# Optimization experiments

Hardware: AMD Instinct MI355X
Metric: run time of the kernel (lower is better)

## Reference

```python
import jax, jax.numpy as jnp
import numpy as np

DIM = 256
B, N, M = 4, 4096, 8


def setup_inputs() -> dict:
    key = jax.random.key(0)
    ks = jax.random.split(key, 12)
    s = 1.0 / np.sqrt(DIM)
    return {
        "q": jax.random.normal(ks[0], (B, DIM, N, M), jnp.float32),
        "k": jax.random.normal(ks[1], (B, DIM, N, M), jnp.float32),
        "pos": jax.random.normal(ks[2], (B, N, M, DIM), jnp.float32),
        "mask": jnp.ones((B, N, M, 1), jnp.int32),
        "Wq": jax.random.normal(ks[3], (DIM, DIM), jnp.float32) * s,
        "Wk": jax.random.normal(ks[4], (DIM, DIM), jnp.float32) * s,
        "Wv": jax.random.normal(ks[5], (DIM, DIM), jnp.float32) * s,
        "W1": jax.random.normal(ks[6], (DIM, DIM // 2), jnp.float32) * s,
        "b1": jnp.zeros((DIM // 2,), jnp.float32),
        "W2": jax.random.normal(ks[7], (DIM // 2, DIM), jnp.float32) * s,
        "b2": jnp.zeros((DIM,), jnp.float32),
        "Wo": jax.random.normal(ks[8], (DIM, DIM), jnp.float32) * s,
        "bo": jnp.zeros((DIM,), jnp.float32),
    }


def reference(q, k, pos, mask, Wq, Wk, Wv, W1, b1, W2, b2, Wo, bo):
    # (B, dim, N, M) -> (B, N, M, dim)
    qh = jnp.einsum('bdnm,de->bnme', q, Wq)
    kh = jnp.einsum('bdnm,de->bnme', k, Wk)
    v = kh @ Wv  # note: v_fc applied to k_fc output, as in the original
    attn = kh - qh + pos
    attn = jax.nn.relu(attn @ W1 + b1) @ W2 + b2
    attn = jnp.where(mask == 0, -1e9, attn)
    attn = jax.nn.sigmoid(attn)
    x = (v + pos) * attn
    x = x @ Wo + bo
    return jnp.transpose(x, (0, 3, 1, 2))  # back to (B, dim, N, M)
```

## Files before the change

### kernel.cpp

```cpp
#include <hip/hip_runtime.h>

#define DIMX 256
#define NMX  32768
#define TB   64

typedef short s16x8 __attribute__((ext_vector_type(8)));
typedef float f32x4 __attribute__((ext_vector_type(4)));

#define OFF_WQN   (0u)
#define OFF_WK    (131072u)
#define OFF_WKV   (262144u)
#define OFF_W1    (393216u)
#define OFF_W2    (458752u)
#define OFF_WO    (524288u)
#define OFF_KVF32 (655360u)

__device__ __forceinline__ ushort f2bf(float f) {
  uint u = __builtin_bit_cast(uint, f);
  return (ushort)((u + 0x7FFFu + ((u >> 16) & 1u)) >> 16);
}

__global__ void wkv_kernel(const float* __restrict__ Wk, const float* __restrict__ Wv,
                           float* __restrict__ outw) {
  const int e = threadIdx.x, d = blockIdx.x;
  float acc = 0.f;
  #pragma unroll 8
  for (int m = 0; m < DIMX; ++m) acc += Wk[d * DIMX + m] * Wv[m * DIMX + e];
  outw[d * DIMX + e] = acc;
}

__global__ void pack_kernel(const float* __restrict__ Wq, const float* __restrict__ Wk,
                            const float* __restrict__ Wkvf, const float* __restrict__ W1,
                            const float* __restrict__ W2, const float* __restrict__ Wo,
                            ushort* __restrict__ wsout) {
  const int fid = blockIdx.x, lane = threadIdx.x;
  const float* src; int Eout = 256; float sgn = 1.f; uint off; int local;
  if (fid < 128)      { src = Wq;   sgn = -1.f; off = OFF_WQN; local = fid;       }
  else if (fid < 256) { src = Wk;   off = OFF_WK;  local = fid - 128;             }
  else if (fid < 384) { src = Wkvf; off = OFF_WKV; local = fid - 256;             }
  else if (fid < 448) { src = W1;   Eout = 128; off = OFF_W1; local = fid - 384;  }
  else if (fid < 512) { src = W2;   off = OFF_W2;  local = fid - 448;             }
  else                { src = Wo;   off = OFF_WO;  local = fid - 512;             }
  const int R  = Eout >> 4;
  const int ks = local / R, r = local - ks * R;
  const int e  = r * 16 + (lane & 15);
  const int k0 = ks * 32 + (lane >> 4) * 8;
  union { uint4 u4; ushort us[8]; } o;
  #pragma unroll
  for (int j = 0; j < 8; ++j) o.us[j] = f2bf(sgn * src[(k0 + j) * Eout + e]);
  *(uint4*)((char*)wsout + off + (((uint)local * 64u + (uint)lane) * 16u)) = o.u4;
}

#define MFMA16(A,B,C) __builtin_amdgcn_mfma_f32_16x16x32_bf16(A, B, C, 0, 0, 0)

__global__ __launch_bounds__(512, 4) void fused_main(
    const float* __restrict__ q, const float* __restrict__ kin,
    const float* __restrict__ pos, const int* __restrict__ mask,
    const float* __restrict__ b1, const float* __restrict__ b2,
    const float* __restrict__ bo, const ushort* __restrict__ wfr,
    float* __restrict__ out)
{
  __shared__ __align__(1024) ushort bufA[TB * DIMX];
  __shared__ __align__(1024) ushort bufB[TB * DIMX];
  const char* wb = (const char*)wfr;

  const int tid = threadIdx.x;
  const int w = tid >> 6, l = tid & 63;
  const int c = l & 15, g = l >> 4;
  const int b  = blockIdx.x >> 9;
  const int t0 = (blockIdx.x & 511) * TB;

  auto ldB = [&](const ushort* buf, int ks, int tf) -> s16x8 {
    const int t = (tf << 4) + c;
    const int col = (ks << 6) + (g << 4);
    return *(const s16x8*)((const char*)buf + t * 512 + (col ^ ((t & 7) << 4)));
  };
  auto ldA = [&](uint moff, int fi) -> s16x8 {
    return *(const s16x8*)(wb + moff + (((uint)fi << 6) | (uint)l) * 16u);
  };
  auto stRow4 = [&](ushort* buf, int e0, int t, uint lo, uint hi) {
    const int byte = t * 512 + (((uint)(e0 * 2)) ^ ((t & 7) << 4));
    *(uint2*)((char*)buf + byte) = uint2{lo, hi};
  };

  {
    const size_t pbase = (size_t)b * DIMX * NMX + t0 + l;
    #pragma unroll 4
    for (int dd = 0; dd < 32; dd += 2) {
      const int d = (w << 5) + dd;
      const float q0 = q[pbase + (size_t)d * NMX];
      const float q1 = q[pbase + (size_t)(d + 1) * NMX];
      const float k0 = kin[pbase + (size_t)d * NMX];
      const float k1 = kin[pbase + (size_t)(d + 1) * NMX];
      const int byte = l * 512 + ((d * 2) ^ ((l & 7) << 4));
      *(uint*)((char*)bufA + byte) = (uint)f2bf(q0) | ((uint)f2bf(q1) << 16);
      *(uint*)((char*)bufB + byte) = (uint)f2bf(k0) | ((uint)f2bf(k1) << 16);
    }
  }
  __syncthreads();

  f32x4 av[2][4];
  #pragma unroll
  for (int ef = 0; ef < 2; ++ef)
    #pragma unroll
    for (int tf = 0; tf < 4; ++tf) av[ef][tf] = f32x4{0.f, 0.f, 0.f, 0.f};
  #pragma unroll 2
  for (int ks = 0; ks < 8; ++ks) {
    const s16x8 a0 = ldA(OFF_WKV, (ks << 4) + (w << 1));
    const s16x8 a1 = ldA(OFF_WKV, (ks << 4) + (w << 1) + 1);
    #pragma unroll
    for (int tf = 0; tf < 4; ++tf) {
      const s16x8 bf = ldB(bufB, ks, tf);
      av[0][tf] = MFMA16(a0, bf, av[0][tf]);
      av[1][tf] = MFMA16(a1, bf, av[1][tf]);
    }
  }
  uint vbf[2][4][2];
  #pragma unroll
  for (int ef = 0; ef < 2; ++ef)
    #pragma unroll
    for (int tf = 0; tf < 4; ++tf)
      #pragma unroll
      for (int p = 0; p < 2; ++p)
        vbf[ef][tf][p] = (uint)f2bf(av[ef][tf][2 * p]) |
                         ((uint)f2bf(av[ef][tf][2 * p + 1]) << 16);

  f32x4 aa[2][4];
  #pragma unroll
  for (int ef = 0; ef < 2; ++ef)
    #pragma unroll
    for (int tf = 0; tf < 4; ++tf) aa[ef][tf] = f32x4{0.f, 0.f, 0.f, 0.f};
  #pragma unroll 2
  for (int ks = 0; ks < 8; ++ks) {
    const s16x8 a0 = ldA(OFF_WQN, (ks << 4) + (w << 1));
    const s16x8 a1 = ldA(OFF_WQN, (ks << 4) + (w << 1) + 1);
    #pragma unroll
    for (int tf = 0; tf < 4; ++tf) {
      const s16x8 bf = ldB(bufA, ks, tf);
      aa[0][tf] = MFMA16(a0, bf, aa[0][tf]);
      aa[1][tf] = MFMA16(a1, bf, aa[1][tf]);
    }
  }
  #pragma unroll 2
  for (int ks = 0; ks < 8; ++ks) {
    const s16x8 a0 = ldA(OFF_WK, (ks << 4) + (w << 1));
    const s16x8 a1 = ldA(OFF_WK, (ks << 4) + (w << 1) + 1);
    #pragma unroll
    for (int tf = 0; tf < 4; ++tf) {
      const s16x8 bf = ldB(bufB, ks, tf);
      aa[0][tf] = MFMA16(a0, bf, aa[0][tf]);
      aa[1][tf] = MFMA16(a1, bf, aa[1][tf]);
    }
  }
  __syncthreads();

  #pragma unroll
  for (int tf = 0; tf < 4; ++tf) {
    const int t = (tf << 4) + c;
    const float* pp = pos + ((size_t)b * NMX + t0 + t) * DIMX;
    #pragma unroll
    for (int ef = 0; ef < 2; ++ef) {
      const int e0 = (w << 5) + (ef << 4) + (g << 2);
      const f32x4 p4 = *(const f32x4*)(pp + e0);
      const uint lo = (uint)f2bf(aa[ef][tf][0] + p4[0]) |
                      ((uint)f2bf(aa[ef][tf][1] + p4[1]) << 16);
      const uint hi = (uint)f2bf(aa[ef][tf][2] + p4[2]) |
                      ((uint)f2bf(aa[ef][tf][3] + p4[3]) << 16);
      stRow4(bufA, e0, t, lo, hi);
    }
  }
  __syncthreads();

  f32x4 ah[4];
  #pragma unroll
  for (int tf = 0; tf < 4; ++tf) ah[tf] = f32x4{0.f, 0.f, 0.f, 0.f};
  #pragma unroll 2
  for (int ks = 0; ks < 8; ++ks) {
    const s16x8 a0 = ldA(OFF_W1, (ks << 3) + w);
    #pragma unroll
    for (int tf = 0; tf < 4; ++tf) {
      const s16x8 bf = ldB(bufA, ks, tf);
      ah[tf] = MFMA16(a0, bf, ah[tf]);
    }
  }
  {
    const int e0 = (w << 4) + (g << 2);
    const f32x4 b1v = *(const f32x4*)(b1 + e0);
    #pragma unroll
    for (int tf = 0; tf < 4; ++tf) {
      const int t = (tf << 4) + c;
      const uint lo = (uint)f2bf(fmaxf(ah[tf][0] + b1v[0], 0.f)) |
                      ((uint)f2bf(fmaxf(ah[tf][1] + b1v[1], 0.f)) << 16);
      const uint hi = (uint)f2bf(fmaxf(ah[tf][2] + b1v[2], 0.f)) |
                      ((uint)f2bf(fmaxf(ah[tf][3] + b1v[3], 0.f)) << 16);
      stRow4(bufB, e0, t, lo, hi);
    }
  }
  __syncthreads();

  f32x4 as[2][4];
  #pragma unroll
  for (int ef = 0; ef < 2; ++ef)
    #pragma unroll
    for (int tf = 0; tf < 4; ++tf) as[ef][tf] = f32x4{0.f, 0.f, 0.f, 0.f};
  #pragma unroll
  for (int ks = 0; ks < 4; ++ks) {
    const s16x8 a0 = ldA(OFF_W2, (ks << 4) + (w << 1));
    const s16x8 a1 = ldA(OFF_W2, (ks << 4) + (w << 1) + 1);
    #pragma unroll
    for (int tf = 0; tf < 4; ++tf) {
      const s16x8 bf = ldB(bufB, ks, tf);
      as[0][tf] = MFMA16(a0, bf, as[0][tf]);
      as[1][tf] = MFMA16(a1, bf, as[1][tf]);
    }
  }
  #pragma unroll
  for (int tf = 0; tf < 4; ++tf) {
    const int t = (tf << 4) + c;
    const int mk = mask[(size_t)b * NMX + t0 + t];
    const float* pp = pos + ((size_t)b * NMX + t0 + t) * DIMX;
    #pragma unroll
    for (int ef = 0; ef < 2; ++ef) {
      const int e0 = (w << 5) + (ef << 4) + (g << 2);
      const f32x4 p4  = *(const f32x4*)(pp + e0);
      const f32x4 b2v = *(const f32x4*)(b2 + e0);
      float xv[4];
      #pragma unroll
      for (int i = 0; i < 4; ++i) {
        float sv = as[ef][tf][i] + b2v[i];
        if (mk == 0) sv = -1e9f;
        const float sig = 1.f / (1.f + __expf(-sv));
        const uint pv = vbf[ef][tf][i >> 1];
        const float vv = (i & 1) ? __builtin_bit_cast(float, pv & 0xffff0000u)
                                 : __builtin_bit_cast(float, pv << 16);
        xv[i] = (vv + p4[i]) * sig;
      }
      const uint lo = (uint)f2bf(xv[0]) | ((uint)f2bf(xv[1]) << 16);
      const uint hi = (uint)f2bf(xv[2]) | ((uint)f2bf(xv[3]) << 16);
      stRow4(bufA, e0, t, lo, hi);
    }
  }
  __syncthreads();

  f32x4 ao[2][4];
  #pragma unroll
  for (int ef = 0; ef < 2; ++ef)
    #pragma unroll
    for (int tf = 0; tf < 4; ++tf) ao[ef][tf] = f32x4{0.f, 0.f, 0.f, 0.f};
  #pragma unroll 2
  for (int ks = 0; ks < 8; ++ks) {
    const s16x8 a0 = ldA(OFF_WO, (ks << 4) + (w << 1));
    const s16x8 a1 = ldA(OFF_WO, (ks << 4) + (w << 1) + 1);
    #pragma unroll
    for (int tf = 0; tf < 4; ++tf) {
      const s16x8 bf = ldB(bufA, ks, tf);
      ao[0][tf] = MFMA16(a0, bf, ao[0][tf]);
      ao[1][tf] = MFMA16(a1, bf, ao[1][tf]);
    }
  }
  #pragma unroll
  for (int ef = 0; ef < 2; ++ef) {
    const int e0 = (w << 5) + (ef << 4) + (g << 2);
    const f32x4 bov = *(const f32x4*)(bo + e0);
    #pragma unroll
    for (int i = 0; i < 4; ++i) {
      float* ob = out + ((size_t)b * DIMX + e0 + i) * NMX + t0 + c;
      #pragma unroll
      for (int tf = 0; tf < 4; ++tf)
        ob[tf << 4] = ao[ef][tf][i] + bov[i];
    }
  }
}

extern "C" void kernel_launch(void* const* d_in, const int* in_sizes, int n_in,
                              void* d_out, int out_size, void* d_ws, size_t ws_size,
                              hipStream_t stream) {
  (void)in_sizes; (void)n_in; (void)out_size; (void)ws_size;
  const float* q   = (const float*)d_in[0];
  const float* k   = (const float*)d_in[1];
  const float* pos = (const float*)d_in[2];
  const int*   msk = (const int*)d_in[3];
  const float* Wq  = (const float*)d_in[4];
  const float* Wk  = (const float*)d_in[5];
  const float* Wv  = (const float*)d_in[6];
  const float* W1  = (const float*)d_in[7];
  const float* b1  = (const float*)d_in[8];
  const float* W2  = (const float*)d_in[9];
  const float* b2  = (const float*)d_in[10];
  const float* Wo  = (const float*)d_in[11];
  const float* bo  = (const float*)d_in[12];
  float* out = (float*)d_out;
  char* ws = (char*)d_ws;
  float*  wkvf = (float*)(ws + OFF_KVF32);
  ushort* wfr  = (ushort*)ws;

  wkv_kernel<<<dim3(256), dim3(256), 0, stream>>>(Wk, Wv, wkvf);
  pack_kernel<<<dim3(640), dim3(64), 0, stream>>>(Wq, Wk, wkvf, W1, W2, Wo, wfr);
  fused_main<<<dim3(2048), dim3(512), 0, stream>>>(q, k, pos, msk, b1, b2, bo, wfr, out);
}
```

Baseline: 206.1 us.

## Shrink LDS footprint by staging q in halves, raise occupancy, use hardware bf16 pack

Replaces the two 32KB LDS buffers with one 32KB main buffer and one 16KB auxiliary buffer. q is now staged in two 128-column halves, with an extra barrier between the halves, so more blocks can fit per CU; launch bounds go from 4 to 6 blocks. The software bf16 rounding is replaced with the v_cvt_pk_bf16_f32 instruction, and staging stores are widened to 16 bytes. pos is kept in registers as packed bf16 instead of being reloaded from global memory, which adds register pressure and slightly lowers the precision of pos in the final product.

```diff
diff --git a/kernel.cpp b/kernel.cpp
--- a/kernel.cpp
+++ b/kernel.cpp
@@ -18,6 +18,18 @@
 __device__ __forceinline__ ushort f2bf(float f) {
   uint u = __builtin_bit_cast(uint, f);
   return (ushort)((u + 0x7FFFu + ((u >> 16) & 1u)) >> 16);
+}
+
+__device__ __forceinline__ uint cvtpk(float lo, float hi) {
+  uint r;
+  asm("v_cvt_pk_bf16_f32 %0, %1, %2" : "=v"(r) : "v"(lo), "v"(hi));
+  return r;
+}
+__device__ __forceinline__ float bf_lo(uint u) {
+  return __builtin_bit_cast(float, u << 16);
+}
+__device__ __forceinline__ float bf_hi(uint u) {
+  return __builtin_bit_cast(float, u & 0xffff0000u);
 }
 
 __global__ void wkv_kernel(const float* __restrict__ Wk, const float* __restrict__ Wv,
@@ -53,15 +65,17 @@
 
 #define MFMA16(A,B,C) __builtin_amdgcn_mfma_f32_16x16x32_bf16(A, B, C, 0, 0, 0)
 
-__global__ __launch_bounds__(512, 4) void fused_main(
+__global__ __launch_bounds__(512, 6) void fused_main(
     const float* __restrict__ q, const float* __restrict__ kin,
     const float* __restrict__ pos, const int* __restrict__ mask,
     const float* __restrict__ b1, const float* __restrict__ b2,
     const float* __restrict__ bo, const ushort* __restrict__ wfr,
     float* __restrict__ out)
 {
-  __shared__ __align__(1024) ushort bufA[TB * DIMX];
-  __shared__ __align__(1024) ushort bufB[TB * DIMX];
+  __shared__ __align__(1024) ushort mainb[TB * DIMX];
+  __shared__ __align__(1024) ushort auxb[TB * (DIMX / 2)];
+  char* mb = (char*)mainb;
+  char* ab = (char*)auxb;
   const char* wb = (const char*)wfr;
 
   const int tid = threadIdx.x;
@@ -70,33 +84,64 @@
   const int b  = blockIdx.x >> 9;
   const int t0 = (blockIdx.x & 511) * TB;
 
-  auto ldB = [&](const ushort* buf, int ks, int tf) -> s16x8 {
+  auto ldBm = [&](int ks, int tf) -> s16x8 {
     const int t = (tf << 4) + c;
     const int col = (ks << 6) + (g << 4);
-    return *(const s16x8*)((const char*)buf + t * 512 + (col ^ ((t & 7) << 4)));
+    return *(const s16x8*)(mb + t * 512 + (col ^ ((t & 7) << 4)));
+  };
+  auto ldBa = [&](int ks, int tf) -> s16x8 {
+    const int t = (tf << 4) + c;
+    const int col = (ks << 6) + (g << 4);
+    return *(const s16x8*)(ab + t * 256 + (col ^ ((t & 7) << 4)));
   };
   auto ldA = [&](uint moff, int fi) -> s16x8 {
     return *(const s16x8*)(wb + moff + (((uint)fi << 6) | (uint)l) * 16u);
   };
-  auto stRow4 = [&](ushort* buf, int e0, int t, uint lo, uint hi) {
+  auto stM4 = [&](int e0, int t, uint lo, uint hi) {
     const int byte = t * 512 + (((uint)(e0 * 2)) ^ ((t & 7) << 4));
-    *(uint2*)((char*)buf + byte) = uint2{lo, hi};
-  };
-
-  {
-    const size_t pbase = (size_t)b * DIMX * NMX + t0 + l;
-    #pragma unroll 4
-    for (int dd = 0; dd < 32; dd += 2) {
-      const int d = (w << 5) + dd;
-      const float q0 = q[pbase + (size_t)d * NMX];
-      const float q1 = q[pbase + (size_t)(d + 1) * NMX];
-      const float k0 = kin[pbase + (size_t)d * NMX];
-      const float k1 = kin[pbase + (size_t)(d + 1) * NMX];
-      const int byte = l * 512 + ((d * 2) ^ ((l & 7) << 4));
-      *(uint*)((char*)bufA + byte) = (uint)f2bf(q0) | ((uint)f2bf(q1) << 16);
-      *(uint*)((char*)bufB + byte) = (uint)f2bf(k0) | ((uint)f2bf(k1) << 16);
-    }
-  }
+    *(uint2*)(mb + byte) = uint2{lo, hi};
+  };
+  auto stA4 = [&](int e0, int t, uint lo, uint hi) {
+    const int byte = t * 256 + (((uint)(e0 * 2)) ^ ((t & 7) << 4));
+    *(uint2*)(ab + byte) = uint2{lo, hi};
+  };
+
+  const size_t gbase = (size_t)b * DIMX * NMX + t0 + l;
+
+  auto stage_k = [&]() {
+    #pragma unroll
+    for (int j4 = 0; j4 < 4; ++j4) {
+      const int d0 = (w << 5) + (j4 << 3);
+      uint pk[4];
+      #pragma unroll
+      for (int p = 0; p < 4; ++p) {
+        const float v0 = kin[gbase + (size_t)(d0 + 2 * p) * NMX];
+        const float v1 = kin[gbase + (size_t)(d0 + 2 * p + 1) * NMX];
+        pk[p] = cvtpk(v0, v1);
+      }
+      const int byte = l * 512 + ((d0 * 2) ^ ((l & 7) << 4));
+      *(uint4*)(mb + byte) = uint4{pk[0], pk[1], pk[2], pk[3]};
+    }
+  };
+  auto stage_qh = [&](int half) {
+    #pragma unroll
+    for (int j4 = 0; j4 < 2; ++j4) {
+      const int dl = (w << 4) + (j4 << 3);
+      const int d  = (half << 7) + dl;
+      uint pk[4];
+      #pragma unroll
+      for (int p = 0; p < 4; ++p) {
+        const float v0 = q[gbase + (size_t)(d + 2 * p) * NMX];
+        const float v1 = q[gbase + (size_t)(d + 2 * p + 1) * NMX];
+        pk[p] = cvtpk(v0, v1);
+      }
+      const int byte = l * 256 + ((dl * 2) ^ ((l & 7) << 4));
+      *(uint4*)(ab + byte) = uint4{pk[0], pk[1], pk[2], pk[3]};
+    }
+  };
+
+  stage_k();
+  stage_qh(0);
   __syncthreads();
 
   f32x4 av[2][4];
@@ -110,7 +155,7 @@
     const s16x8 a1 = ldA(OFF_WKV, (ks << 4) + (w << 1) + 1);
     #pragma unroll
     for (int tf = 0; tf < 4; ++tf) {
-      const s16x8 bf = ldB(bufB, ks, tf);
+      const s16x8 bf = ldBm(ks, tf);
       av[0][tf] = MFMA16(a0, bf, av[0][tf]);
       av[1][tf] = MFMA16(a1, bf, av[1][tf]);
     }
@@ -119,41 +164,57 @@
   #pragma unroll
   for (int ef = 0; ef < 2; ++ef)
     #pragma unroll
-    for (int tf = 0; tf < 4; ++tf)
-      #pragma unroll
-      for (int p = 0; p < 2; ++p)
-        vbf[ef][tf][p] = (uint)f2bf(av[ef][tf][2 * p]) |
-                         ((uint)f2bf(av[ef][tf][2 * p + 1]) << 16);
+    for (int tf = 0; tf < 4; ++tf) {
+      vbf[ef][tf][0] = cvtpk(av[ef][tf][0], av[ef][tf][1]);
+      vbf[ef][tf][1] = cvtpk(av[ef][tf][2], av[ef][tf][3]);
+    }
 
   f32x4 aa[2][4];
   #pragma unroll
   for (int ef = 0; ef < 2; ++ef)
     #pragma unroll
     for (int tf = 0; tf < 4; ++tf) aa[ef][tf] = f32x4{0.f, 0.f, 0.f, 0.f};
-  #pragma unroll 2
-  for (int ks = 0; ks < 8; ++ks) {
-    const s16x8 a0 = ldA(OFF_WQN, (ks << 4) + (w << 1));
-    const s16x8 a1 = ldA(OFF_WQN, (ks << 4) + (w << 1) + 1);
-    #pragma unroll
-    for (int tf = 0; tf < 4; ++tf) {
-      const s16x8 bf = ldB(bufA, ks, tf);
-      aa[0][tf] = MFMA16(a0, bf, aa[0][tf]);
-      aa[1][tf] = MFMA16(a1, bf, aa[1][tf]);
-    }
-  }
   #pragma unroll 2
   for (int ks = 0; ks < 8; ++ks) {
     const s16x8 a0 = ldA(OFF_WK, (ks << 4) + (w << 1));
     const s16x8 a1 = ldA(OFF_WK, (ks << 4) + (w << 1) + 1);
     #pragma unroll
     for (int tf = 0; tf < 4; ++tf) {
-      const s16x8 bf = ldB(bufB, ks, tf);
+      const s16x8 bf = ldBm(ks, tf);
       aa[0][tf] = MFMA16(a0, bf, aa[0][tf]);
       aa[1][tf] = MFMA16(a1, bf, aa[1][tf]);
     }
   }
-  __syncthreads();
-
+
+  #pragma unroll 2
+  for (int ks = 0; ks < 4; ++ks) {
+    const s16x8 a0 = ldA(OFF_WQN, (ks << 4) + (w << 1));
+    const s16x8 a1 = ldA(OFF_WQN, (ks << 4) + (w << 1) + 1);
+    #pragma unroll
+    for (int tf = 0; tf < 4; ++tf) {
+      const s16x8 bf = ldBa(ks, tf);
+      aa[0][tf] = MFMA16(a0, bf, aa[0][tf]);
+      aa[1][tf] = MFMA16(a1, bf, aa[1][tf]);
+    }
+  }
+  __syncthreads();
+
+  stage_qh(1);
+  __syncthreads();
+
+  #pragma unroll 2
+  for (int ks = 4; ks < 8; ++ks) {
+    const s16x8 a0 = ldA(OFF_WQN, (ks << 4) + (w << 1));
+    const s16x8 a1 = ldA(OFF_WQN, (ks << 4) + (w << 1) + 1);
+    #pragma unroll
+    for (int tf = 0; tf < 4; ++tf) {
+      const s16x8 bf = ldBa(ks - 4, tf);
+      aa[0][tf] = MFMA16(a0, bf, aa[0][tf]);
+      aa[1][tf] = MFMA16(a1, bf, aa[1][tf]);
+    }
+  }
+
+  uint posbf[2][4][2];
   #pragma unroll
   for (int tf = 0; tf < 4; ++tf) {
     const int t = (tf << 4) + c;
@@ -162,11 +223,11 @@
     for (int ef = 0; ef < 2; ++ef) {
       const int e0 = (w << 5) + (ef << 4) + (g << 2);
       const f32x4 p4 = *(const f32x4*)(pp + e0);
-      const uint lo = (uint)f2bf(aa[ef][tf][0] + p4[0]) |
-                      ((uint)f2bf(aa[ef][tf][1] + p4[1]) << 16);
-      const uint hi = (uint)f2bf(aa[ef][tf][2] + p4[2]) |
-                      ((uint)f2bf(aa[ef][tf][3] + p4[3]) << 16);
-      stRow4(bufA, e0, t, lo, hi);
+      posbf[ef][tf][0] = cvtpk(p4[0], p4[1]);
+      posbf[ef][tf][1] = cvtpk(p4[2], p4[3]);
+      const uint lo = cvtpk(aa[ef][tf][0] + p4[0], aa[ef][tf][1] + p4[1]);
+      const uint hi = cvtpk(aa[ef][tf][2] + p4[2], aa[ef][tf][3] + p4[3]);
+      stM4(e0, t, lo, hi);
     }
   }
   __syncthreads();
@@ -179,7 +240,7 @@
     const s16x8 a0 = ldA(OFF_W1, (ks << 3) + w);
     #pragma unroll
     for (int tf = 0; tf < 4; ++tf) {
-      const s16x8 bf = ldB(bufA, ks, tf);
+      const s16x8 bf = ldBm(ks, tf);
       ah[tf] = MFMA16(a0, bf, ah[tf]);
     }
   }
@@ -189,11 +250,11 @@
     #pragma unroll
     for (int tf = 0; tf < 4; ++tf) {
       const int t = (tf << 4) + c;
-      const uint lo = (uint)f2bf(fmaxf(ah[tf][0] + b1v[0], 0.f)) |
-                      ((uint)f2bf(fmaxf(ah[tf][1] + b1v[1], 0.f)) << 16);
-      const uint hi = (uint)f2bf(fmaxf(ah[tf][2] + b1v[2], 0.f)) |
-                      ((uint)f2bf(fmaxf(ah[tf][3] + b1v[3], 0.f)) << 16);
-      stRow4(bufB, e0, t, lo, hi);
+      const uint lo = cvtpk(fmaxf(ah[tf][0] + b1v[0], 0.f),
+                            fmaxf(ah[tf][1] + b1v[1], 0.f));
+      const uint hi = cvtpk(fmaxf(ah[tf][2] + b1v[2], 0.f),
+                            fmaxf(ah[tf][3] + b1v[3], 0.f));
+      stA4(e0, t, lo, hi);
     }
   }
   __syncthreads();
@@ -209,7 +270,7 @@
     const s16x8 a1 = ldA(OFF_W2, (ks << 4) + (w << 1) + 1);
     #pragma unroll
     for (int tf = 0; tf < 4; ++tf) {
-      const s16x8 bf = ldB(bufB, ks, tf);
+      const s16x8 bf = ldBa(ks, tf);
       as[0][tf] = MFMA16(a0, bf, as[0][tf]);
       as[1][tf] = MFMA16(a1, bf, as[1][tf]);
     }
@@ -218,11 +279,9 @@
   for (int tf = 0; tf < 4; ++tf) {
     const int t = (tf << 4) + c;
     const int mk = mask[(size_t)b * NMX + t0 + t];
-    const float* pp = pos + ((size_t)b * NMX + t0 + t) * DIMX;
     #pragma unroll
     for (int ef = 0; ef < 2; ++ef) {
       const int e0 = (w << 5) + (ef << 4) + (g << 2);
-      const f32x4 p4  = *(const f32x4*)(pp + e0);
       const f32x4 b2v = *(const f32x4*)(b2 + e0);
       float xv[4];
       #pragma unroll
@@ -231,13 +290,12 @@
         if (mk == 0) sv = -1e9f;
         const float sig = 1.f / (1.f + __expf(-sv));
         const uint pv = vbf[ef][tf][i >> 1];
-        const float vv = (i & 1) ? __builtin_bit_cast(float, pv & 0xffff0000u)
-                                 : __builtin_bit_cast(float, pv << 16);
-        xv[i] = (vv + p4[i]) * sig;
+        const uint pp = posbf[ef][tf][i >> 1];
+        const float vv = (i & 1) ? bf_hi(pv) : bf_lo(pv);
+        const float pf = (i & 1) ? bf_hi(pp) : bf_lo(pp);
+        xv[i] = (vv + pf) * sig;
       }
-      const uint lo = (uint)f2bf(xv[0]) | ((uint)f2bf(xv[1]) << 16);
-      const uint hi = (uint)f2bf(xv[2]) | ((uint)f2bf(xv[3]) << 16);
-      stRow4(bufA, e0, t, lo, hi);
+      stM4(e0, t, cvtpk(xv[0], xv[1]), cvtpk(xv[2], xv[3]));
     }
   }
   __syncthreads();
@@ -253,7 +311,7 @@
     const s16x8 a1 = ldA(OFF_WO, (ks << 4) + (w << 1) + 1);
     #pragma unroll
     for (int tf = 0; tf < 4; ++tf) {
-      const s16x8 bf = ldB(bufA, ks, tf);
+      const s16x8 bf = ldBm(ks, tf);
       ao[0][tf] = MFMA16(a0, bf, ao[0][tf]);
       ao[1][tf] = MFMA16(a1, bf, ao[1][tf]);
     }
```

Measured after the change: 218.1 us. 1.06x slower.
